# Kernel optimization log

Hardware: AMD Instinct MI355X
Metric: run time of the kernel (lower is better)

The kernel has to match this reference:

```python
import jax, jax.numpy as jnp
import numpy as np
from jax import lax

B, A, C, M = 8, 100000, 80, 32
ALPHA, GAMMA = 0.25, 2.0


def _calc_iou(a, b):
    # a: [A,4] anchors, b: [M,4] gt boxes -> [A,M]
    area = (b[:, 2] - b[:, 0]) * (b[:, 3] - b[:, 1])
    iw = jnp.clip(jnp.minimum(a[:, None, 2], b[None, :, 2]) - jnp.maximum(a[:, None, 0], b[None, :, 0]), 0.0)
    ih = jnp.clip(jnp.minimum(a[:, None, 3], b[None, :, 3]) - jnp.maximum(a[:, None, 1], b[None, :, 1]), 0.0)
    inter = iw * ih
    ua = jnp.clip(((a[:, 2] - a[:, 0]) * (a[:, 3] - a[:, 1]))[:, None] + area[None, :] - inter, 1e-8)
    return inter / ua


def _per_image(cls_p, reg, ann, anchor):
    # cls_p: [A,C], reg: [A,4], ann: [M,9], anchor: [A,4]
    p = jnp.clip(cls_p, 1e-4, 1.0 - 1e-4)
    iou = _calc_iou(anchor, ann[:, :4])            # [A,M]
    iou_max = jnp.max(iou, axis=1)                 # [A]
    iou_arg = jnp.argmax(iou, axis=1)              # [A]
    assigned = ann[iou_arg]                        # [A,9]
    pos = iou_max >= 0.5
    num_pos = jnp.sum(pos)

    # targets: -1 = ignore, 0 = background, one-hot for positives
    t = jnp.where(iou_max[:, None] < 0.4, 0.0, -1.0)
    cls_idx = lax.stop_gradient(assigned[:, 4]).astype(jnp.int32)
    t = jnp.where(pos[:, None], jax.nn.one_hot(cls_idx, C, dtype=p.dtype), t)

    alpha_f = jnp.where(t == 1.0, ALPHA, 1.0 - ALPHA)
    fw = jnp.where(t == 1.0, 1.0 - p, p)
    bce = -(t * jnp.log(p) + (1.0 - t) * jnp.log(1.0 - p))
    cls_loss = jnp.where(t != -1.0, alpha_f * fw ** GAMMA * bce, 0.0)
    cls_l = jnp.sum(cls_loss) / jnp.maximum(num_pos.astype(p.dtype), 1.0)

    aw = anchor[:, 2] - anchor[:, 0]
    ah = anchor[:, 3] - anchor[:, 1]
    acx = anchor[:, 0] + 0.5 * aw
    acy = anchor[:, 1] + 0.5 * ah
    gw_raw = assigned[:, 2] - assigned[:, 0]
    gh_raw = assigned[:, 3] - assigned[:, 1]
    gcx = assigned[:, 0] + 0.5 * gw_raw
    gcy = assigned[:, 1] + 0.5 * gh_raw
    gw = jnp.clip(gw_raw, 1.0)
    gh = jnp.clip(gh_raw, 1.0)
    tgt = jnp.stack([(gcx - acx) / aw, (gcy - acy) / ah,
                     jnp.log(gw / aw), jnp.log(gh / ah)], axis=1)
    tgt = tgt / jnp.array([0.1, 0.1, 0.2, 0.2], dtype=p.dtype)
    diff = jnp.abs(tgt - reg)
    sl1 = jnp.where(diff <= 1.0 / 9.0, 0.5 * 9.0 * diff ** 2, diff - 0.5 / 9.0)
    denom = jnp.maximum(num_pos.astype(p.dtype) * 4.0, 1.0)
    reg_l = jnp.where(num_pos > 0,
                      jnp.sum(jnp.where(pos[:, None], sl1, 0.0)) / denom,
                      jnp.zeros((), p.dtype))
    return cls_l, reg_l


def setup_inputs() -> dict:
    key = jax.random.key(0)
    k = jax.random.split(key, 8)
    classifications = jax.random.uniform(k[0], (B, A, C), jnp.float32, 1e-3, 1.0 - 1e-3)
    regressions = 0.1 * jax.random.normal(k[1], (B, A, 4), jnp.float32)
    ax0 = jax.random.uniform(k[2], (A,), jnp.float32, 0.0, 900.0)
    ay0 = jax.random.uniform(k[3], (A,), jnp.float32, 0.0, 900.0)
    awh = jax.random.uniform(k[4], (A, 2), jnp.float32, 16.0, 128.0)
    anchors = jnp.stack([ax0, ay0, ax0 + awh[:, 0], ay0 + awh[:, 1]], axis=1)[None]
    b0 = jax.random.uniform(k[5], (B, M, 2), jnp.float32, 0.0, 800.0)
    bwh = jax.random.uniform(k[6], (B, M, 2), jnp.float32, 8.0, 200.0)
    labels = jax.random.randint(k[7], (B, M, 1), 0, C).astype(jnp.float32)
    extra = jnp.zeros((B, M, 4), jnp.float32)  # cols 5..8: instance id + geo filler
    annotations = jnp.concatenate([b0, b0 + bwh, labels, extra], axis=-1)  # [B,M,9]
    return dict(classifications=classifications, regressions=regressions,
                anchors=anchors, annotations=annotations)


def reference(classifications, regressions, anchors, annotations):
    anchor = anchors[0]
    cls_l, reg_l = jax.vmap(_per_image, in_axes=(0, 0, 0, None))(
        classifications, regressions, annotations, anchor)
    return jnp.stack([jnp.mean(cls_l), jnp.mean(reg_l)])
```

## Files before the change

kernel.cpp:

```cpp
#include <hip/hip_runtime.h>

#define A_N 100000
#define B_N 8
#define C_N 80
#define M_N 32

typedef float vfloat4 __attribute__((ext_vector_type(4)));


__device__ __forceinline__ float bg_s4(vfloat4 v) {
    float p0 = fminf(fmaxf(v.x, 1e-4f), 1.0f - 1e-4f);
    float p1 = fminf(fmaxf(v.y, 1e-4f), 1.0f - 1e-4f);
    float p2 = fminf(fmaxf(v.z, 1e-4f), 1.0f - 1e-4f);
    float p3 = fminf(fmaxf(v.w, 1e-4f), 1.0f - 1e-4f);
    float l0 = __logf(1.0f - p0);
    float l1 = __logf(1.0f - p1);
    float l2 = __logf(1.0f - p2);
    float l3 = __logf(1.0f - p3);
    return fmaf(p0 * p0, l0, fmaf(p1 * p1, l1, fmaf(p2 * p2, l2, p3 * p3 * l3)));
}

__global__ __launch_bounds__(256) void focal_main(
    const vfloat4* __restrict__ cls4,
    const float*  __restrict__ clsf,
    const float4* __restrict__ reg4,
    const float4* __restrict__ anc4,
    const float*  __restrict__ ann,
    float* __restrict__ cls_sum, float* __restrict__ reg_sum, int* __restrict__ npos)
{
    __shared__ float annL[M_N][6];
    __shared__ float scaleL[256];
    __shared__ float redA[4];
    __shared__ float redB[4];
    __shared__ int   redI[4];

    const int b   = blockIdx.y;
    const int a0  = blockIdx.x * 256;
    const int tid = threadIdx.x;

    for (int i = tid; i < M_N * 5; i += 256) {
        int m = i / 5, c = i % 5;
        annL[m][c] = ann[(b * M_N + m) * 9 + c];
    }
    __syncthreads();
    if (tid < M_N) {
        annL[tid][5] = (annL[tid][2] - annL[tid][0]) * (annL[tid][3] - annL[tid][1]);
    }
    __syncthreads();

    const int a = a0 + tid;
    const bool valid = a < A_N;
    const int nA = min(256, A_N - a0);
    const bool full = (nA == 256);
    const vfloat4* cbase = cls4 + ((size_t)b * A_N + a0) * 20;

    float4 an = anc4[valid ? a : A_N - 1];

    vfloat4 bufA[10], bufB[10];
    if (full) {
        #pragma unroll
        for (int u = 0; u < 10; ++u)
            bufA[u] = __builtin_nontemporal_load(cbase + tid + (u << 8));
        #pragma unroll
        for (int u = 0; u < 10; ++u)
            bufB[u] = __builtin_nontemporal_load(cbase + tid + ((u + 10) << 8));
    }

    float aw = an.z - an.x, ah = an.w - an.y;
    float aArea = aw * ah;
    float best = -1.0f; int bidx = 0;
    #pragma unroll 8
    for (int m = 0; m < M_N; ++m) {
        float iw = fminf(an.z, annL[m][2]) - fmaxf(an.x, annL[m][0]);
        float ih = fminf(an.w, annL[m][3]) - fmaxf(an.y, annL[m][1]);
        iw = fmaxf(iw, 0.0f); ih = fmaxf(ih, 0.0f);
        float inter = iw * ih;
        float ua = fmaxf(aArea + annL[m][5] - inter, 1e-8f);
        float iou = inter / ua;
        if (iou > best) { best = iou; bidx = m; }
    }
    const bool pos = valid && (best >= 0.5f);
    const int  st  = valid ? (pos ? 2 : (best < 0.4f ? 0 : 1)) : 1;
    scaleL[tid] = (st != 1) ? -0.75f : 0.0f;
    __syncthreads();

    float clsacc = 0.0f;
    if (full) {
        #pragma unroll
        for (int u = 0; u < 10; ++u) {
            int i = tid + (u << 8);
            clsacc = fmaf(scaleL[i / 20], bg_s4(bufA[u]), clsacc);
        }
        #pragma unroll
        for (int u = 0; u < 10; ++u) {
            int i = tid + ((u + 10) << 8);
            clsacc = fmaf(scaleL[i / 20], bg_s4(bufB[u]), clsacc);
        }
    } else {
        const int n4 = nA * 20;
        for (int i = tid; i < n4; i += 256) {
            vfloat4 v = __builtin_nontemporal_load(cbase + i);
            clsacc = fmaf(scaleL[i / 20], bg_s4(v), clsacc);
        }
    }

    float regacc = 0.0f;
    const unsigned long long bal = __ballot(pos);
    if (bal) {
        if (pos) {
            float4 r = reg4[(size_t)b * A_N + a];
            float gx0 = annL[bidx][0], gy0 = annL[bidx][1];
            float gx1 = annL[bidx][2], gy1 = annL[bidx][3];
            float gwr = gx1 - gx0, ghr = gy1 - gy0;
            float gcx = gx0 + 0.5f * gwr, gcy = gy0 + 0.5f * ghr;
            float gw = fmaxf(gwr, 1.0f), gh = fmaxf(ghr, 1.0f);
            float acx = an.x + 0.5f * aw, acy = an.y + 0.5f * ah;
            float t0 = (gcx - acx) / aw * 10.0f;
            float t1 = (gcy - acy) / ah * 10.0f;
            float t2 = __logf(gw / aw) * 5.0f;
            float t3 = __logf(gh / ah) * 5.0f;
            float d0 = fabsf(t0 - r.x), d1 = fabsf(t1 - r.y);
            float d2 = fabsf(t2 - r.z), d3 = fabsf(t3 - r.w);
            const float th = 1.0f / 9.0f;
            const float hs = 0.5f / 9.0f;
            regacc  = (d0 <= th) ? 4.5f * d0 * d0 : d0 - hs;
            regacc += (d1 <= th) ? 4.5f * d1 * d1 : d1 - hs;
            regacc += (d2 <= th) ? 4.5f * d2 * d2 : d2 - hs;
            regacc += (d3 <= th) ? 4.5f * d3 * d3 : d3 - hs;

            int ci = (int)annL[bidx][4];
            float pc = clsf[((size_t)b * A_N + a) * C_N + ci];
            pc = fminf(fmaxf(pc, 1e-4f), 1.0f - 1e-4f);
            float qc = 1.0f - pc;
            clsacc += -0.25f * qc * qc * __logf(pc) + 0.75f * pc * pc * __logf(qc);
        }
    }

    #pragma unroll
    for (int o = 32; o > 0; o >>= 1) {
        regacc += __shfl_down(regacc, o, 64);
        clsacc += __shfl_down(clsacc, o, 64);
    }
    const int lane = tid & 63, wid = tid >> 6;
    if (lane == 0) { redA[wid] = regacc; redB[wid] = clsacc; redI[wid] = __popcll(bal); }
    __syncthreads();
    if (tid == 0) {
        float rs = redA[0] + redA[1] + redA[2] + redA[3];
        float cs = redB[0] + redB[1] + redB[2] + redB[3];
        int   np = redI[0] + redI[1] + redI[2] + redI[3];
        if (rs != 0.0f) atomicAdd(&reg_sum[b], rs);
        if (np)         atomicAdd(&npos[b], np);
        atomicAdd(&cls_sum[b], cs);
    }
}

__global__ void focal_finalize(const float* __restrict__ cls_sum,
                               const float* __restrict__ reg_sum,
                               const int* __restrict__ npos,
                               float* __restrict__ out)
{
    if (threadIdx.x == 0) {
        float c = 0.0f, r = 0.0f;
        for (int b = 0; b < B_N; ++b) {
            float np = (float)npos[b];
            c += cls_sum[b] / fmaxf(np, 1.0f);
            r += (npos[b] > 0) ? reg_sum[b] / (4.0f * np) : 0.0f;
        }
        out[0] = c / (float)B_N;
        out[1] = r / (float)B_N;
    }
}

extern "C" void kernel_launch(void* const* d_in, const int* in_sizes, int n_in,
                              void* d_out, int out_size, void* d_ws, size_t ws_size,
                              hipStream_t stream) {
    const float* cls = (const float*)d_in[0];
    const float* reg = (const float*)d_in[1];
    const float* anc = (const float*)d_in[2];
    const float* ann = (const float*)d_in[3];

    float* ws      = (float*)d_ws;
    float* cls_sum = ws;
    float* reg_sum = ws + 8;
    int*   npos    = (int*)(ws + 16);

    (void)hipMemsetAsync(d_ws, 0, 24 * sizeof(float), stream);

    dim3 grid((A_N + 255) / 256, B_N);
    focal_main<<<grid, 256, 0, stream>>>(
        (const vfloat4*)cls, cls, (const float4*)reg, (const float4*)anc, ann,
        cls_sum, reg_sum, npos);

    focal_finalize<<<1, 64, 0, stream>>>(cls_sum, reg_sum, npos, (float*)d_out);
}
```

Baseline: 398.6 us.

## Make classification reduction wave-local with shuffles instead of block shared scale

Each wave now streams the classification rows for its own 64 anchors and fetches per-anchor scales from its lanes with __shfl, removing the shared scaleL buffer and a block-wide barrier. Loads of the classification data are issued after the IoU computation rather than before it, with the second batch overlapped with the first batch's math. The annotation preload is simplified to one thread per box. This drops a block-level sync but also removes the early prefetch that previously overlapped the loads with the IoU loop, and adds 20 shuffles per lane.

```diff
diff --git a/kernel.cpp b/kernel.cpp
--- a/kernel.cpp
+++ b/kernel.cpp
@@ -29,42 +29,31 @@
     float* __restrict__ cls_sum, float* __restrict__ reg_sum, int* __restrict__ npos)
 {
     __shared__ float annL[M_N][6];
-    __shared__ float scaleL[256];
     __shared__ float redA[4];
     __shared__ float redB[4];
     __shared__ int   redI[4];
 
-    const int b   = blockIdx.y;
-    const int a0  = blockIdx.x * 256;
-    const int tid = threadIdx.x;
+    const int b    = blockIdx.y;
+    const int a0   = blockIdx.x * 256;
+    const int tid  = threadIdx.x;
+    const int lane = tid & 63;
+    const int wid  = tid >> 6;
 
-    for (int i = tid; i < M_N * 5; i += 256) {
-        int m = i / 5, c = i % 5;
-        annL[m][c] = ann[(b * M_N + m) * 9 + c];
-    }
-    __syncthreads();
     if (tid < M_N) {
-        annL[tid][5] = (annL[tid][2] - annL[tid][0]) * (annL[tid][3] - annL[tid][1]);
+        const float* ar = ann + ((size_t)b * M_N + tid) * 9;
+        float x0 = ar[0], y0 = ar[1], x1 = ar[2], y1 = ar[3], lb = ar[4];
+        annL[tid][0] = x0; annL[tid][1] = y0;
+        annL[tid][2] = x1; annL[tid][3] = y1;
+        annL[tid][4] = lb; annL[tid][5] = (x1 - x0) * (y1 - y0);
     }
     __syncthreads();
 
-    const int a = a0 + tid;
+    const int aw0   = a0 + (wid << 6);
+    const int a     = aw0 + lane;
     const bool valid = a < A_N;
-    const int nA = min(256, A_N - a0);
-    const bool full = (nA == 256);
-    const vfloat4* cbase = cls4 + ((size_t)b * A_N + a0) * 20;
+    const int vA    = min(64, A_N - aw0);
 
-    float4 an = anc4[valid ? a : A_N - 1];
-
-    vfloat4 bufA[10], bufB[10];
-    if (full) {
-        #pragma unroll
-        for (int u = 0; u < 10; ++u)
-            bufA[u] = __builtin_nontemporal_load(cbase + tid + (u << 8));
-        #pragma unroll
-        for (int u = 0; u < 10; ++u)
-            bufB[u] = __builtin_nontemporal_load(cbase + tid + ((u + 10) << 8));
-    }
+    float4 an = anc4[valid ? a : (A_N - 1)];
 
     float aw = an.z - an.x, ah = an.w - an.y;
     float aArea = aw * ah;
@@ -81,30 +70,10 @@
     }
     const bool pos = valid && (best >= 0.5f);
     const int  st  = valid ? (pos ? 2 : (best < 0.4f ? 0 : 1)) : 1;
-    scaleL[tid] = (st != 1) ? -0.75f : 0.0f;
-    __syncthreads();
-
-    float clsacc = 0.0f;
-    if (full) {
-        #pragma unroll
-        for (int u = 0; u < 10; ++u) {
-            int i = tid + (u << 8);
-            clsacc = fmaf(scaleL[i / 20], bg_s4(bufA[u]), clsacc);
-        }
-        #pragma unroll
-        for (int u = 0; u < 10; ++u) {
-            int i = tid + ((u + 10) << 8);
-            clsacc = fmaf(scaleL[i / 20], bg_s4(bufB[u]), clsacc);
-        }
-    } else {
-        const int n4 = nA * 20;
-        for (int i = tid; i < n4; i += 256) {
-            vfloat4 v = __builtin_nontemporal_load(cbase + i);
-            clsacc = fmaf(scaleL[i / 20], bg_s4(v), clsacc);
-        }
-    }
+    const float myscale = (st != 1) ? -0.75f : 0.0f;
 
     float regacc = 0.0f;
+    float clsacc = 0.0f;
     const unsigned long long bal = __ballot(pos);
     if (bal) {
         if (pos) {
@@ -132,7 +101,37 @@
             float pc = clsf[((size_t)b * A_N + a) * C_N + ci];
             pc = fminf(fmaxf(pc, 1e-4f), 1.0f - 1e-4f);
             float qc = 1.0f - pc;
-            clsacc += -0.25f * qc * qc * __logf(pc) + 0.75f * pc * pc * __logf(qc);
+            clsacc = -0.25f * qc * qc * __logf(pc) + 0.75f * pc * pc * __logf(qc);
+        }
+    }
+
+    if (vA >= 64) {
+        const vfloat4* wbase = cls4 + ((size_t)b * A_N + aw0) * 20;
+
+        vfloat4 bufA[10], bufB[10];
+        #pragma unroll
+        for (int u = 0; u < 10; ++u)
+            bufA[u] = __builtin_nontemporal_load(wbase + (u << 6) + lane);
+
+        float sc[20];
+        #pragma unroll
+        for (int u = 0; u < 20; ++u)
+            sc[u] = __shfl(myscale, ((u << 6) + lane) / 20, 64);
+
+        #pragma unroll
+        for (int u = 0; u < 10; ++u) {
+            bufB[u] = __builtin_nontemporal_load(wbase + ((u + 10) << 6) + lane);
+            clsacc = fmaf(sc[u], bg_s4(bufA[u]), clsacc);
+        }
+        #pragma unroll
+        for (int u = 0; u < 10; ++u)
+            clsacc = fmaf(sc[u + 10], bg_s4(bufB[u]), clsacc);
+    } else if (vA > 0) {
+        const vfloat4* wbase = cls4 + ((size_t)b * A_N + aw0) * 20;
+        const int n4 = vA * 20;
+        for (int i = lane; i < n4; i += 64) {
+            float s = __shfl(myscale, i / 20, 64);
+            clsacc = fmaf(s, bg_s4(__builtin_nontemporal_load(wbase + i)), clsacc);
         }
     }
 
@@ -141,7 +140,6 @@
         regacc += __shfl_down(regacc, o, 64);
         clsacc += __shfl_down(clsacc, o, 64);
     }
-    const int lane = tid & 63, wid = tid >> 6;
     if (lane == 0) { redA[wid] = regacc; redB[wid] = clsacc; redI[wid] = __popcll(bal); }
     __syncthreads();
     if (tid == 0) {
```

New measurement: 380.4 us (median of 2 runs). -4.6%, faster.
